# Kernel tuning notes

Hardware: AMD Instinct MI355X
Metric: run time of the kernel (lower is better)

The kernel has to match this reference:

```python
import jax, jax.numpy as jnp
import numpy as np

BETA = 0.95
THETA = 1.0  # snn.Leaky default threshold
SLOPE = 25.0  # fast_sigmoid surrogate slope

@jax.custom_vjp
def spike_fn(v):
    # Heaviside forward, fast-sigmoid surrogate backward (snntorch surrogate.fast_sigmoid)
    return (v > 0).astype(v.dtype)

def _spike_fwd(v):
    return spike_fn(v), v

def _spike_bwd(v, g):
    return (g / (SLOPE * jnp.abs(v) + 1.0) ** 2,)

spike_fn.defvjp(_spike_fwd, _spike_bwd)


def setup_inputs() -> dict:
    key = jax.random.key(0)
    k = jax.random.split(key, 5)
    T, B, n_in, n_hid, n_out = 500, 256, 96, 64, 80  # n_out = 4 classes * 20 pop
    x = jax.random.uniform(k[0], (T, B, n_in), dtype=jnp.float32)
    s1 = 1.0 / np.sqrt(n_in)
    s2 = 1.0 / np.sqrt(n_hid)
    W1 = jax.random.uniform(k[1], (n_in, n_hid), jnp.float32, -s1, s1)
    b1 = jax.random.uniform(k[2], (n_hid,), jnp.float32, -s1, s1)
    W2 = jax.random.uniform(k[3], (n_hid, n_out), jnp.float32, -s2, s2)
    b2 = jax.random.uniform(k[4], (n_out,), jnp.float32, -s2, s2)
    return {"x": x, "W1": W1, "b1": b1, "W2": W2, "b2": b2}


def reference(x, W1, b1, W2, b2):
    # Dropout is in eval mode (identity). snntorch Leaky with reset_mechanism='subtract':
    #   reset_t = spk_{t-1};  mem_t = beta*mem_{t-1} + cur_t - reset_t*theta;  spk_t = H(mem_t - theta)
    B = x.shape[1]
    n_hid = W1.shape[1]
    n_out = W2.shape[1]
    z_h = jnp.zeros((B, n_hid), x.dtype)
    z_o = jnp.zeros((B, n_out), x.dtype)

    def step(carry, xt):
        mem1, spk1, mem2, spk2 = carry
        cur1 = xt @ W1 + b1
        mem1 = BETA * mem1 + cur1 - spk1 * THETA
        spk1 = spike_fn(mem1 - THETA)
        cur2 = spk1 @ W2 + b2
        mem2 = BETA * mem2 + cur2 - spk2 * THETA
        spk2 = spike_fn(mem2 - THETA)
        return (mem1, spk1, mem2, spk2), (spk2, mem2)

    _, (spk_out, mem_out) = jax.lax.scan(step, (z_h, z_h, z_o, z_o), x)
    return spk_out, mem_out
```

## Files before the change

### kernel.cpp

```cpp
#include <hip/hip_runtime.h>


#define T_STEPS 500
#define BATCH   256
#define N_IN    96
#define N_HID   64
#define N_OUT   80
#define CH      50
#define MASK_OFF 8192000

__global__ __launch_bounds__(256) void k1_cur1(
    const float* __restrict__ x,
    const float* __restrict__ W1,
    const float* __restrict__ b1,
    float* __restrict__ cur1)
{
    const int tp   = blockIdx.x >> 2;
    const int b0   = (blockIdx.x & 3) << 6;
    const int t0   = tp * 2;
    const int lane = threadIdx.x & 63;
    const int w    = threadIdx.x >> 6;
    const int o0   = w << 4;

    __shared__ float sm[18944];

    {
        const float4* __restrict__ s0 =
            reinterpret_cast<const float4*>(x + ((size_t)t0 * BATCH + b0) * N_IN);
        const float4* __restrict__ s1 =
            reinterpret_cast<const float4*>(x + ((size_t)(t0 + 1) * BATCH + b0) * N_IN);
        #pragma unroll
        for (int ii = 0; ii < 6; ++ii) {
            const int i = ii * 256 + threadIdx.x;
            const float4 v0 = s0[i], v1 = s1[i];
            const int row = i / 24, g = i % 24;
            *reinterpret_cast<float4*>(&sm[row * 100 + g * 4]) = v0;
            *reinterpret_cast<float4*>(&sm[6400 + row * 100 + g * 4]) = v1;
        }
        const float4* __restrict__ srcw = reinterpret_cast<const float4*>(W1);
        #pragma unroll
        for (int ii = 0; ii < 6; ++ii) {
            const int i = ii * 256 + threadIdx.x;
            *reinterpret_cast<float4*>(&sm[12800 + i * 4]) = srcw[i];
        }
    }
    __syncthreads();

    float acc0[16], acc1[16];
    #pragma unroll
    for (int o = 0; o < 16; ++o) { acc0[o] = 0.0f; acc1[o] = 0.0f; }

    const int xb = lane * 100;
    #pragma unroll 2
    for (int kg = 0; kg < 24; ++kg) {
        const float4 xv0 = *reinterpret_cast<const float4*>(&sm[xb + kg * 4]);
        const float4 xv1 = *reinterpret_cast<const float4*>(&sm[6400 + xb + kg * 4]);
        const float xq0[4] = {xv0.x, xv0.y, xv0.z, xv0.w};
        const float xq1[4] = {xv1.x, xv1.y, xv1.z, xv1.w};
        #pragma unroll
        for (int jj = 0; jj < 4; ++jj) {
            const int k = kg * 4 + jj;
            const float4* __restrict__ wr =
                reinterpret_cast<const float4*>(&sm[12800 + k * 64 + o0]);
            const float4 w0 = wr[0], w1 = wr[1], w2 = wr[2], w3 = wr[3];
            const float xs0 = xq0[jj], xs1 = xq1[jj];
            acc0[0]  = __fmaf_rn(xs0, w0.x, acc0[0]);
            acc0[1]  = __fmaf_rn(xs0, w0.y, acc0[1]);
            acc0[2]  = __fmaf_rn(xs0, w0.z, acc0[2]);
            acc0[3]  = __fmaf_rn(xs0, w0.w, acc0[3]);
            acc0[4]  = __fmaf_rn(xs0, w1.x, acc0[4]);
            acc0[5]  = __fmaf_rn(xs0, w1.y, acc0[5]);
            acc0[6]  = __fmaf_rn(xs0, w1.z, acc0[6]);
            acc0[7]  = __fmaf_rn(xs0, w1.w, acc0[7]);
            acc0[8]  = __fmaf_rn(xs0, w2.x, acc0[8]);
            acc0[9]  = __fmaf_rn(xs0, w2.y, acc0[9]);
            acc0[10] = __fmaf_rn(xs0, w2.z, acc0[10]);
            acc0[11] = __fmaf_rn(xs0, w2.w, acc0[11]);
            acc0[12] = __fmaf_rn(xs0, w3.x, acc0[12]);
            acc0[13] = __fmaf_rn(xs0, w3.y, acc0[13]);
            acc0[14] = __fmaf_rn(xs0, w3.z, acc0[14]);
            acc0[15] = __fmaf_rn(xs0, w3.w, acc0[15]);
            acc1[0]  = __fmaf_rn(xs1, w0.x, acc1[0]);
            acc1[1]  = __fmaf_rn(xs1, w0.y, acc1[1]);
            acc1[2]  = __fmaf_rn(xs1, w0.z, acc1[2]);
            acc1[3]  = __fmaf_rn(xs1, w0.w, acc1[3]);
            acc1[4]  = __fmaf_rn(xs1, w1.x, acc1[4]);
            acc1[5]  = __fmaf_rn(xs1, w1.y, acc1[5]);
            acc1[6]  = __fmaf_rn(xs1, w1.z, acc1[6]);
            acc1[7]  = __fmaf_rn(xs1, w1.w, acc1[7]);
            acc1[8]  = __fmaf_rn(xs1, w2.x, acc1[8]);
            acc1[9]  = __fmaf_rn(xs1, w2.y, acc1[9]);
            acc1[10] = __fmaf_rn(xs1, w2.z, acc1[10]);
            acc1[11] = __fmaf_rn(xs1, w2.w, acc1[11]);
            acc1[12] = __fmaf_rn(xs1, w3.x, acc1[12]);
            acc1[13] = __fmaf_rn(xs1, w3.y, acc1[13]);
            acc1[14] = __fmaf_rn(xs1, w3.z, acc1[14]);
            acc1[15] = __fmaf_rn(xs1, w3.w, acc1[15]);
        }
    }

    __syncthreads();
    #pragma unroll
    for (int o4 = 0; o4 < 4; ++o4) {
        float4 v0, v1;
        v0.x = __fadd_rn(acc0[o4 * 4 + 0], b1[o0 + o4 * 4 + 0]);
        v0.y = __fadd_rn(acc0[o4 * 4 + 1], b1[o0 + o4 * 4 + 1]);
        v0.z = __fadd_rn(acc0[o4 * 4 + 2], b1[o0 + o4 * 4 + 2]);
        v0.w = __fadd_rn(acc0[o4 * 4 + 3], b1[o0 + o4 * 4 + 3]);
        v1.x = __fadd_rn(acc1[o4 * 4 + 0], b1[o0 + o4 * 4 + 0]);
        v1.y = __fadd_rn(acc1[o4 * 4 + 1], b1[o0 + o4 * 4 + 1]);
        v1.z = __fadd_rn(acc1[o4 * 4 + 2], b1[o0 + o4 * 4 + 2]);
        v1.w = __fadd_rn(acc1[o4 * 4 + 3], b1[o0 + o4 * 4 + 3]);
        *reinterpret_cast<float4*>(&sm[lane * 68 + o0 + o4 * 4]) = v0;
        *reinterpret_cast<float4*>(&sm[6400 + lane * 68 + o0 + o4 * 4]) = v1;
    }
    __syncthreads();
    {
        float4* __restrict__ d0 =
            reinterpret_cast<float4*>(cur1 + ((size_t)t0 * BATCH + b0) * N_HID);
        float4* __restrict__ d1 =
            reinterpret_cast<float4*>(cur1 + ((size_t)(t0 + 1) * BATCH + b0) * N_HID);
        #pragma unroll
        for (int ii = 0; ii < 4; ++ii) {
            const int i = ii * 256 + threadIdx.x;
            const int row = i / 16, g = i % 16;
            d0[i] = *reinterpret_cast<const float4*>(&sm[row * 68 + g * 4]);
            d1[i] = *reinterpret_cast<const float4*>(&sm[6400 + row * 68 + g * 4]);
        }
    }
}

__global__ __launch_bounds__(64) void k2_rec1(
    const float* __restrict__ cs,
    unsigned long long* __restrict__ masks)
{
    const int b = blockIdx.x;
    const int h = threadIdx.x;
    const size_t str  = (size_t)BATCH * N_HID;
    const size_t base = (size_t)b * N_HID + h;

    float A[CH], Bv[CH];
    #pragma unroll
    for (int i = 0; i < CH; ++i) A[i] = cs[(size_t)i * str + base];

    float mem = 0.f, s = 0.f;
    unsigned mlo = 0u, mhi = 0u;
    for (int cp = 0; cp < 5; ++cp) {
        const int c0 = 2 * cp;
        #pragma unroll
        for (int i = 0; i < CH; ++i)
            Bv[i] = cs[(size_t)((c0 + 1) * CH + i) * str + base];
        #pragma unroll
        for (int i = 0; i < CH; ++i) {
            const float m = __fsub_rn(__fadd_rn(__fmul_rn(0.95f, mem), A[i]), s);
            mem = m; s = (m > 1.0f) ? 1.0f : 0.0f;
            const unsigned long long bal = __ballot(m > 1.0f);
            mlo = (h == i) ? (unsigned)bal : mlo;
            mhi = (h == i) ? (unsigned)(bal >> 32) : mhi;
        }
        if (h < CH)
            masks[(size_t)(c0 * CH + h) * BATCH + b] =
                ((unsigned long long)mhi << 32) | mlo;
        if (cp < 4) {
            #pragma unroll
            for (int i = 0; i < CH; ++i)
                A[i] = cs[(size_t)((c0 + 2) * CH + i) * str + base];
        }
        #pragma unroll
        for (int i = 0; i < CH; ++i) {
            const float m = __fsub_rn(__fadd_rn(__fmul_rn(0.95f, mem), Bv[i]), s);
            mem = m; s = (m > 1.0f) ? 1.0f : 0.0f;
            const unsigned long long bal = __ballot(m > 1.0f);
            mlo = (h == i) ? (unsigned)bal : mlo;
            mhi = (h == i) ? (unsigned)(bal >> 32) : mhi;
        }
        if (h < CH)
            masks[(size_t)((c0 + 1) * CH + h) * BATCH + b] =
                ((unsigned long long)mhi << 32) | mlo;
    }
}

__global__ __launch_bounds__(256) void k3_cur2(
    const unsigned long long* __restrict__ masks,
    const float* __restrict__ W2,
    const float* __restrict__ b2,
    float* __restrict__ cur2)
{
    const int tq   = blockIdx.x >> 2;
    const int b0   = (blockIdx.x & 3) << 6;
    const int t0   = tq * 4;
    const int lane = threadIdx.x & 63;
    const int w    = threadIdx.x >> 6;
    const int o0   = w * 20;

    __shared__ float ws[64 * 80];

    {
        const float4* __restrict__ srcw = reinterpret_cast<const float4*>(W2);
        #pragma unroll
        for (int ii = 0; ii < 5; ++ii) {
            const int i = ii * 256 + threadIdx.x;
            *reinterpret_cast<float4*>(&ws[i * 4]) = srcw[i];
        }
    }

    unsigned long long mk0, mk1, mk2, mk3;
    mk0 = masks[(size_t)(t0 + 0) * BATCH + b0 + lane];
    mk1 = masks[(size_t)(t0 + 1) * BATCH + b0 + lane];
    mk2 = masks[(size_t)(t0 + 2) * BATCH + b0 + lane];
    mk3 = masks[(size_t)(t0 + 3) * BATCH + b0 + lane];
    __syncthreads();

    float acc0[20], acc1[20], acc2[20], acc3[20];
    #pragma unroll
    for (int o = 0; o < 20; ++o) {
        acc0[o] = 0.0f; acc1[o] = 0.0f; acc2[o] = 0.0f; acc3[o] = 0.0f;
    }

    #pragma unroll 2
    for (int kg = 0; kg < 16; ++kg) {
        #pragma unroll
        for (int jj = 0; jj < 4; ++jj) {
            const int k = kg * 4 + jj;
            const float4* __restrict__ wr =
                reinterpret_cast<const float4*>(&ws[k * 80 + o0]);
            const float4 w0 = wr[0], w1 = wr[1], w2 = wr[2], w3 = wr[3], w4 = wr[4];
            const float wv[20] = {w0.x, w0.y, w0.z, w0.w,
                                  w1.x, w1.y, w1.z, w1.w,
                                  w2.x, w2.y, w2.z, w2.w,
                                  w3.x, w3.y, w3.z, w3.w,
                                  w4.x, w4.y, w4.z, w4.w};
            const float s0 = (float)((mk0 >> k) & 1ULL);
            const float s1 = (float)((mk1 >> k) & 1ULL);
            const float s2 = (float)((mk2 >> k) & 1ULL);
            const float s3 = (float)((mk3 >> k) & 1ULL);
            #pragma unroll
            for (int o = 0; o < 20; ++o) {
                acc0[o] = __fmaf_rn(s0, wv[o], acc0[o]);
                acc1[o] = __fmaf_rn(s1, wv[o], acc1[o]);
                acc2[o] = __fmaf_rn(s2, wv[o], acc2[o]);
                acc3[o] = __fmaf_rn(s3, wv[o], acc3[o]);
            }
        }
    }

    #pragma unroll
    for (int o4 = 0; o4 < 5; ++o4) {
        const float bb0 = b2[o0 + o4 * 4 + 0], bb1 = b2[o0 + o4 * 4 + 1];
        const float bb2 = b2[o0 + o4 * 4 + 2], bb3 = b2[o0 + o4 * 4 + 3];
        float4 v;
        float* d;
        v.x = __fadd_rn(acc0[o4 * 4 + 0], bb0);
        v.y = __fadd_rn(acc0[o4 * 4 + 1], bb1);
        v.z = __fadd_rn(acc0[o4 * 4 + 2], bb2);
        v.w = __fadd_rn(acc0[o4 * 4 + 3], bb3);
        d = cur2 + ((size_t)(t0 + 0) * BATCH + b0 + lane) * N_OUT + o0;
        reinterpret_cast<float4*>(d)[o4] = v;
        v.x = __fadd_rn(acc1[o4 * 4 + 0], bb0);
        v.y = __fadd_rn(acc1[o4 * 4 + 1], bb1);
        v.z = __fadd_rn(acc1[o4 * 4 + 2], bb2);
        v.w = __fadd_rn(acc1[o4 * 4 + 3], bb3);
        d = cur2 + ((size_t)(t0 + 1) * BATCH + b0 + lane) * N_OUT + o0;
        reinterpret_cast<float4*>(d)[o4] = v;
        v.x = __fadd_rn(acc2[o4 * 4 + 0], bb0);
        v.y = __fadd_rn(acc2[o4 * 4 + 1], bb1);
        v.z = __fadd_rn(acc2[o4 * 4 + 2], bb2);
        v.w = __fadd_rn(acc2[o4 * 4 + 3], bb3);
        d = cur2 + ((size_t)(t0 + 2) * BATCH + b0 + lane) * N_OUT + o0;
        reinterpret_cast<float4*>(d)[o4] = v;
        v.x = __fadd_rn(acc3[o4 * 4 + 0], bb0);
        v.y = __fadd_rn(acc3[o4 * 4 + 1], bb1);
        v.z = __fadd_rn(acc3[o4 * 4 + 2], bb2);
        v.w = __fadd_rn(acc3[o4 * 4 + 3], bb3);
        d = cur2 + ((size_t)(t0 + 3) * BATCH + b0 + lane) * N_OUT + o0;
        reinterpret_cast<float4*>(d)[o4] = v;
    }
}

__global__ __launch_bounds__(80) void k4_rec2(float* cm, float* os)
{
    const int b = blockIdx.x;
    const int o = threadIdx.x;
    const size_t str  = (size_t)BATCH * N_OUT;
    const size_t base = (size_t)b * N_OUT + o;

    float A[CH], Bv[CH];
    #pragma unroll
    for (int i = 0; i < CH; ++i) A[i] = cm[(size_t)i * str + base];

    float mem = 0.f, s = 0.f;
    for (int cp = 0; cp < 5; ++cp) {
        const int c0 = 2 * cp;
        #pragma unroll
        for (int i = 0; i < CH; ++i)
            Bv[i] = cm[(size_t)((c0 + 1) * CH + i) * str + base];
        #pragma unroll
        for (int i = 0; i < CH; ++i) {
            const int t = c0 * CH + i;
            const float m = __fsub_rn(__fadd_rn(__fmul_rn(0.95f, mem), A[i]), s);
            mem = m; s = (m > 1.0f) ? 1.0f : 0.0f;
            os[(size_t)t * str + base] = s;
            cm[(size_t)t * str + base] = m;
        }
        if (cp < 4) {
            #pragma unroll
            for (int i = 0; i < CH; ++i)
                A[i] = cm[(size_t)((c0 + 2) * CH + i) * str + base];
        }
        #pragma unroll
        for (int i = 0; i < CH; ++i) {
            const int t = (c0 + 1) * CH + i;
            const float m = __fsub_rn(__fadd_rn(__fmul_rn(0.95f, mem), Bv[i]), s);
            mem = m; s = (m > 1.0f) ? 1.0f : 0.0f;
            os[(size_t)t * str + base] = s;
            cm[(size_t)t * str + base] = m;
        }
    }
}

extern "C" void kernel_launch(void* const* d_in, const int* in_sizes, int n_in,
                              void* d_out, int out_size, void* d_ws, size_t ws_size,
                              hipStream_t stream) {
    const float* x  = (const float*)d_in[0];
    const float* W1 = (const float*)d_in[1];
    const float* b1 = (const float*)d_in[2];
    const float* W2 = (const float*)d_in[3];
    const float* b2 = (const float*)d_in[4];
    float* outs = (float*)d_out;
    float* outm = outs + (size_t)T_STEPS * BATCH * N_OUT;
    unsigned long long* masks =
        (unsigned long long*)(outs + MASK_OFF);

    k1_cur1<<<250 * 4, 256, 0, stream>>>(x, W1, b1, outs);
    k2_rec1<<<BATCH, 64, 0, stream>>>(outs, masks);
    k3_cur2<<<125 * 4, 256, 0, stream>>>(masks, W2, b2, outm);
    k4_rec2<<<BATCH, 80, 0, stream>>>(outm, outs);
}
```

Measured before the change: 98.98 us.

## Compute four timesteps per block in cur1 GEMM with double-buffered K-chunks

The input-projection kernel now processes four timesteps per block instead of two, so each W1 tile read from shared memory feeds four x rows. The grid is halved to match. The x tile is loaded in K-chunks of 24 into two alternating shared buffers, with the next chunk's global load issued while the current chunk is being computed. This raises register pressure to 64 accumulators and uses narrower strided global loads, and leaves fewer blocks to spread across the CUs.

```diff
diff --git a/kernel.cpp b/kernel.cpp
--- a/kernel.cpp
+++ b/kernel.cpp
@@ -15,117 +15,113 @@
     const float* __restrict__ b1,
     float* __restrict__ cur1)
 {
-    const int tp   = blockIdx.x >> 2;
+    const int tq   = blockIdx.x >> 2;
     const int b0   = (blockIdx.x & 3) << 6;
-    const int t0   = tp * 2;
+    const int t0   = tq * 4;
     const int lane = threadIdx.x & 63;
     const int w    = threadIdx.x >> 6;
     const int o0   = w << 4;
 
-    __shared__ float sm[18944];
+    __shared__ float sm[18432];
+    const int XS0 = 0, XS1 = 6144, WS = 12288;
 
     {
-        const float4* __restrict__ s0 =
-            reinterpret_cast<const float4*>(x + ((size_t)t0 * BATCH + b0) * N_IN);
-        const float4* __restrict__ s1 =
-            reinterpret_cast<const float4*>(x + ((size_t)(t0 + 1) * BATCH + b0) * N_IN);
+        const float4* __restrict__ srcw = reinterpret_cast<const float4*>(W1);
         #pragma unroll
         for (int ii = 0; ii < 6; ++ii) {
             const int i = ii * 256 + threadIdx.x;
-            const float4 v0 = s0[i], v1 = s1[i];
-            const int row = i / 24, g = i % 24;
-            *reinterpret_cast<float4*>(&sm[row * 100 + g * 4]) = v0;
-            *reinterpret_cast<float4*>(&sm[6400 + row * 100 + g * 4]) = v1;
-        }
-        const float4* __restrict__ srcw = reinterpret_cast<const float4*>(W1);
+            *reinterpret_cast<float4*>(&sm[WS + i * 4]) = srcw[i];
+        }
         #pragma unroll
         for (int ii = 0; ii < 6; ++ii) {
-            const int i = ii * 256 + threadIdx.x;
-            *reinterpret_cast<float4*>(&sm[12800 + i * 4]) = srcw[i];
+            const int i   = ii * 256 + threadIdx.x;
+            const int row = i / 6, g = i % 6;
+            const int p   = row >> 6, bb = row & 63;
+            const float4 v = *reinterpret_cast<const float4*>(
+                x + ((size_t)(t0 + p) * BATCH + b0 + bb) * N_IN + g * 4);
+            *reinterpret_cast<float4*>(&sm[XS0 + row * 24 + g * 4]) = v;
         }
     }
     __syncthreads();
 
-    float acc0[16], acc1[16];
-    #pragma unroll
-    for (int o = 0; o < 16; ++o) { acc0[o] = 0.0f; acc1[o] = 0.0f; }
-
-    const int xb = lane * 100;
-    #pragma unroll 2
-    for (int kg = 0; kg < 24; ++kg) {
-        const float4 xv0 = *reinterpret_cast<const float4*>(&sm[xb + kg * 4]);
-        const float4 xv1 = *reinterpret_cast<const float4*>(&sm[6400 + xb + kg * 4]);
-        const float xq0[4] = {xv0.x, xv0.y, xv0.z, xv0.w};
-        const float xq1[4] = {xv1.x, xv1.y, xv1.z, xv1.w};
-        #pragma unroll
-        for (int jj = 0; jj < 4; ++jj) {
-            const int k = kg * 4 + jj;
-            const float4* __restrict__ wr =
-                reinterpret_cast<const float4*>(&sm[12800 + k * 64 + o0]);
-            const float4 w0 = wr[0], w1 = wr[1], w2 = wr[2], w3 = wr[3];
-            const float xs0 = xq0[jj], xs1 = xq1[jj];
-            acc0[0]  = __fmaf_rn(xs0, w0.x, acc0[0]);
-            acc0[1]  = __fmaf_rn(xs0, w0.y, acc0[1]);
-            acc0[2]  = __fmaf_rn(xs0, w0.z, acc0[2]);
-            acc0[3]  = __fmaf_rn(xs0, w0.w, acc0[3]);
-            acc0[4]  = __fmaf_rn(xs0, w1.x, acc0[4]);
-            acc0[5]  = __fmaf_rn(xs0, w1.y, acc0[5]);
-            acc0[6]  = __fmaf_rn(xs0, w1.z, acc0[6]);
-            acc0[7]  = __fmaf_rn(xs0, w1.w, acc0[7]);
-            acc0[8]  = __fmaf_rn(xs0, w2.x, acc0[8]);
-            acc0[9]  = __fmaf_rn(xs0, w2.y, acc0[9]);
-            acc0[10] = __fmaf_rn(xs0, w2.z, acc0[10]);
-            acc0[11] = __fmaf_rn(xs0, w2.w, acc0[11]);
-            acc0[12] = __fmaf_rn(xs0, w3.x, acc0[12]);
-            acc0[13] = __fmaf_rn(xs0, w3.y, acc0[13]);
-            acc0[14] = __fmaf_rn(xs0, w3.z, acc0[14]);
-            acc0[15] = __fmaf_rn(xs0, w3.w, acc0[15]);
-            acc1[0]  = __fmaf_rn(xs1, w0.x, acc1[0]);
-            acc1[1]  = __fmaf_rn(xs1, w0.y, acc1[1]);
-            acc1[2]  = __fmaf_rn(xs1, w0.z, acc1[2]);
-            acc1[3]  = __fmaf_rn(xs1, w0.w, acc1[3]);
-            acc1[4]  = __fmaf_rn(xs1, w1.x, acc1[4]);
-            acc1[5]  = __fmaf_rn(xs1, w1.y, acc1[5]);
-            acc1[6]  = __fmaf_rn(xs1, w1.z, acc1[6]);
-            acc1[7]  = __fmaf_rn(xs1, w1.w, acc1[7]);
-            acc1[8]  = __fmaf_rn(xs1, w2.x, acc1[8]);
-            acc1[9]  = __fmaf_rn(xs1, w2.y, acc1[9]);
-            acc1[10] = __fmaf_rn(xs1, w2.z, acc1[10]);
-            acc1[11] = __fmaf_rn(xs1, w2.w, acc1[11]);
-            acc1[12] = __fmaf_rn(xs1, w3.x, acc1[12]);
-            acc1[13] = __fmaf_rn(xs1, w3.y, acc1[13]);
-            acc1[14] = __fmaf_rn(xs1, w3.z, acc1[14]);
-            acc1[15] = __fmaf_rn(xs1, w3.w, acc1[15]);
-        }
-    }
-
+    float acc[4][16];
+    #pragma unroll
+    for (int p = 0; p < 4; ++p)
+        #pragma unroll
+        for (int o = 0; o < 16; ++o) acc[p][o] = 0.0f;
+
+    #pragma unroll 1
+    for (int c = 0; c < 4; ++c) {
+        const int rd = (c & 1) ? XS1 : XS0;
+        const int wr_ = (c & 1) ? XS0 : XS1;
+
+        if (c < 3) {
+            #pragma unroll
+            for (int ii = 0; ii < 6; ++ii) {
+                const int i   = ii * 256 + threadIdx.x;
+                const int row = i / 6, g = i % 6;
+                const int p   = row >> 6, bb = row & 63;
+                const float4 v = *reinterpret_cast<const float4*>(
+                    x + ((size_t)(t0 + p) * BATCH + b0 + bb) * N_IN
+                      + (c + 1) * 24 + g * 4);
+                *reinterpret_cast<float4*>(&sm[wr_ + row * 24 + g * 4]) = v;
+            }
+        }
+
+        #pragma unroll
+        for (int kg = 0; kg < 6; ++kg) {
+            float4 xv0 = *reinterpret_cast<const float4*>(&sm[rd + (0 * 64 + lane) * 24 + kg * 4]);
+            float4 xv1 = *reinterpret_cast<const float4*>(&sm[rd + (1 * 64 + lane) * 24 + kg * 4]);
+            float4 xv2 = *reinterpret_cast<const float4*>(&sm[rd + (2 * 64 + lane) * 24 + kg * 4]);
+            float4 xv3 = *reinterpret_cast<const float4*>(&sm[rd + (3 * 64 + lane) * 24 + kg * 4]);
+            const float xq[4][4] = {{xv0.x, xv0.y, xv0.z, xv0.w},
+                                    {xv1.x, xv1.y, xv1.z, xv1.w},
+                                    {xv2.x, xv2.y, xv2.z, xv2.w},
+                                    {xv3.x, xv3.y, xv3.z, xv3.w}};
+            #pragma unroll
+            for (int jj = 0; jj < 4; ++jj) {
+                const int k = c * 24 + kg * 4 + jj;
+                const float4* __restrict__ wvp =
+                    reinterpret_cast<const float4*>(&sm[WS + k * 64 + o0]);
+                const float4 w0 = wvp[0], w1 = wvp[1], w2 = wvp[2], w3 = wvp[3];
+                const float wv[16] = {w0.x, w0.y, w0.z, w0.w,
+                                      w1.x, w1.y, w1.z, w1.w,
+                                      w2.x, w2.y, w2.z, w2.w,
+                                      w3.x, w3.y, w3.z, w3.w};
+                #pragma unroll
+                for (int p = 0; p < 4; ++p) {
+                    const float xs = xq[p][jj];
+                    #pragma unroll
+                    for (int o = 0; o < 16; ++o)
+                        acc[p][o] = __fmaf_rn(xs, wv[o], acc[p][o]);
+                }
+            }
+        }
+        __syncthreads();
+    }
+
+    #pragma unroll
+    for (int p = 0; p < 4; ++p) {
+        #pragma unroll
+        for (int o4 = 0; o4 < 4; ++o4) {
+            float4 v;
+            v.x = __fadd_rn(acc[p][o4 * 4 + 0], b1[o0 + o4 * 4 + 0]);
+            v.y = __fadd_rn(acc[p][o4 * 4 + 1], b1[o0 + o4 * 4 + 1]);
+            v.z = __fadd_rn(acc[p][o4 * 4 + 2], b1[o0 + o4 * 4 + 2]);
+            v.w = __fadd_rn(acc[p][o4 * 4 + 3], b1[o0 + o4 * 4 + 3]);
+            *reinterpret_cast<float4*>(&sm[p * 4352 + lane * 68 + o0 + o4 * 4]) = v;
+        }
+    }
     __syncthreads();
     #pragma unroll
-    for (int o4 = 0; o4 < 4; ++o4) {
-        float4 v0, v1;
-        v0.x = __fadd_rn(acc0[o4 * 4 + 0], b1[o0 + o4 * 4 + 0]);
-        v0.y = __fadd_rn(acc0[o4 * 4 + 1], b1[o0 + o4 * 4 + 1]);
-        v0.z = __fadd_rn(acc0[o4 * 4 + 2], b1[o0 + o4 * 4 + 2]);
-        v0.w = __fadd_rn(acc0[o4 * 4 + 3], b1[o0 + o4 * 4 + 3]);
-        v1.x = __fadd_rn(acc1[o4 * 4 + 0], b1[o0 + o4 * 4 + 0]);
-        v1.y = __fadd_rn(acc1[o4 * 4 + 1], b1[o0 + o4 * 4 + 1]);
-        v1.z = __fadd_rn(acc1[o4 * 4 + 2], b1[o0 + o4 * 4 + 2]);
-        v1.w = __fadd_rn(acc1[o4 * 4 + 3], b1[o0 + o4 * 4 + 3]);
-        *reinterpret_cast<float4*>(&sm[lane * 68 + o0 + o4 * 4]) = v0;
-        *reinterpret_cast<float4*>(&sm[6400 + lane * 68 + o0 + o4 * 4]) = v1;
-    }
-    __syncthreads();
-    {
-        float4* __restrict__ d0 =
-            reinterpret_cast<float4*>(cur1 + ((size_t)t0 * BATCH + b0) * N_HID);
-        float4* __restrict__ d1 =
-            reinterpret_cast<float4*>(cur1 + ((size_t)(t0 + 1) * BATCH + b0) * N_HID);
+    for (int p = 0; p < 4; ++p) {
+        float4* __restrict__ dst = reinterpret_cast<float4*>(
+            cur1 + ((size_t)(t0 + p) * BATCH + b0) * N_HID);
         #pragma unroll
         for (int ii = 0; ii < 4; ++ii) {
             const int i = ii * 256 + threadIdx.x;
             const int row = i / 16, g = i % 16;
-            d0[i] = *reinterpret_cast<const float4*>(&sm[row * 68 + g * 4]);
-            d1[i] = *reinterpret_cast<const float4*>(&sm[6400 + row * 68 + g * 4]);
+            dst[i] = *reinterpret_cast<const float4*>(&sm[p * 4352 + row * 68 + g * 4]);
         }
     }
 }
@@ -331,7 +327,7 @@
     unsigned long long* masks =
         (unsigned long long*)(outs + MASK_OFF);
 
-    k1_cur1<<<250 * 4, 256, 0, stream>>>(x, W1, b1, outs);
+    k1_cur1<<<125 * 4, 256, 0, stream>>>(x, W1, b1, outs);
     k2_rec1<<<BATCH, 64, 0, stream>>>(outs, masks);
     k3_cur2<<<125 * 4, 256, 0, stream>>>(masks, W2, b2, outm);
     k4_rec2<<<BATCH, 80, 0, stream>>>(outm, outs);
```

New measurement: 99.41 us. Within noise of the previous version (+0.4%).
